# Performance work log

Measured on AMD Instinct MI355X. Metric: run time of the kernel, lower is better.

## Reference

```python
import jax, jax.numpy as jnp
import numpy as np

HIDDEN = 768
NUM_HEADS = 12
HEAD_DIM = HIDDEN // NUM_HEADS


def setup_inputs() -> dict:
    key = jax.random.key(0)
    ks = jax.random.split(key, 10)
    B, S = 4, 2048
    scale = 1.0 / np.sqrt(HIDDEN)
    inp = {
        "hidden_states": jax.random.normal(ks[0], (B, S, HIDDEN), dtype=jnp.float32),
        "attention_mask": jnp.ones((B, S), dtype=jnp.float32),
        "Wq": jax.random.normal(ks[1], (HIDDEN, HIDDEN), dtype=jnp.float32) * scale,
        "bq": jnp.zeros((HIDDEN,), dtype=jnp.float32),
        "Wk": jax.random.normal(ks[2], (HIDDEN, HIDDEN), dtype=jnp.float32) * scale,
        "bk": jnp.zeros((HIDDEN,), dtype=jnp.float32),
        "Wv": jax.random.normal(ks[3], (HIDDEN, HIDDEN), dtype=jnp.float32) * scale,
        "bv": jnp.zeros((HIDDEN,), dtype=jnp.float32),
        "Wo": jax.random.normal(ks[4], (HIDDEN, HIDDEN), dtype=jnp.float32) * scale,
        "bo": jnp.zeros((HIDDEN,), dtype=jnp.float32),
    }
    return inp


def _split_heads(x):
    # [B,S,H] -> [B,nh,S,dh]
    B, S, _ = x.shape
    return x.reshape(B, S, NUM_HEADS, HEAD_DIM).transpose(0, 2, 1, 3)


def reference(hidden_states, attention_mask, Wq, bq, Wk, bk, Wv, bv, Wo, bo):
    # Linear projections (torch nn.Linear: x @ W.T + b; here W stored as [in,out])
    q = _split_heads(hidden_states @ Wq + bq)
    k = _split_heads(hidden_states @ Wk + bk)
    v = _split_heads(hidden_states @ Wv + bv)

    # scores: [B,nh,S,S]
    scores = jnp.einsum("bhqd,bhkd->bhqk", q, k) / np.sqrt(HEAD_DIM).astype(np.float32)

    # outer-product mask: [B,1,S,S], broadcast over heads
    ext = (attention_mask[:, :, None] * attention_mask[:, None, :])[:, None, :, :]
    scores = ext * scores - (1.0 - ext) * 1e9

    probs = jax.nn.softmax(scores, axis=-1)
    ctx = jnp.einsum("bhqk,bhkd->bhqd", probs, v)  # [B,nh,S,dh]
    B, _, S, _ = ctx.shape
    ctx = ctx.transpose(0, 2, 1, 3).reshape(B, S, HIDDEN)
    out = ctx @ Wo + bo
    # torch F.gelu default: exact (erf-based)
    return jax.nn.gelu(out, approximate=False)
```

## Files before the change

### kernel.cpp

```cpp
#include <hip/hip_runtime.h>
#include <math.h>

#define HIDDEN 768
#define NH 12
#define DH 64
#define SEQ 2048
#define BATCH 4

typedef __bf16 bf16;
typedef bf16 bf16x4 __attribute__((ext_vector_type(4)));
typedef bf16 bf16x8 __attribute__((ext_vector_type(8)));
typedef float f32x4 __attribute__((ext_vector_type(4)));

__global__ __launch_bounds__(256) void prep_x(const float* __restrict__ X,
                                              bf16* __restrict__ Xb) {
    const size_t i = ((size_t)blockIdx.x * 256 + threadIdx.x) * 8;
    float4 a = *(const float4*)(X + i);
    float4 b = *(const float4*)(X + i + 4);
    bf16x8 o = {(bf16)a.x, (bf16)a.y, (bf16)a.z, (bf16)a.w,
                (bf16)b.x, (bf16)b.y, (bf16)b.z, (bf16)b.w};
    *(bf16x8*)(Xb + i) = o;
}

__global__ __launch_bounds__(256) void prep_w(const float* __restrict__ Wq,
                                              const float* __restrict__ Wk,
                                              const float* __restrict__ Wv,
                                              const float* __restrict__ Wo,
                                              bf16* __restrict__ Wt,
                                              bf16* __restrict__ Wot_hi,
                                              bf16* __restrict__ Wot_lo) {
    __shared__ float Ts[64][68];
    const int tid = threadIdx.x;
    const int n0 = blockIdx.x * 64, k0 = blockIdx.y * 64, z = blockIdx.z;
    const float* W = (z == 0) ? Wq : (z == 1) ? Wk : (z == 2) ? Wv : Wo;

    {
        const int r = tid >> 2, c = (tid & 3) << 4;
        const float* src = W + (size_t)(k0 + r) * HIDDEN + n0 + c;
#pragma unroll
        for (int j = 0; j < 4; ++j)
            *(float4*)&Ts[r][c + 4 * j] = *(const float4*)(src + 4 * j);
    }
    __syncthreads();

    const int nl = tid >> 2, kc = (tid & 3) << 4;
    float v[16];
#pragma unroll
    for (int j = 0; j < 16; ++j) v[j] = Ts[kc + j][nl];

    if (z < 3) {
        bf16 hi[16];
#pragma unroll
        for (int j = 0; j < 16; ++j) hi[j] = (bf16)v[j];
        const size_t off = (size_t)(z * HIDDEN + n0 + nl) * HIDDEN + k0 + kc;
        *(bf16x8*)(Wt + off) = *(bf16x8*)&hi[0];
        *(bf16x8*)(Wt + off + 8) = *(bf16x8*)&hi[8];
    } else {
        bf16 hi[16], lo[16];
#pragma unroll
        for (int j = 0; j < 16; ++j) {
            hi[j] = (bf16)v[j];
            lo[j] = (bf16)(v[j] - (float)hi[j]);
        }
        const size_t off = (size_t)(n0 + nl) * HIDDEN + k0 + kc;
        *(bf16x8*)(Wot_hi + off) = *(bf16x8*)&hi[0];
        *(bf16x8*)(Wot_hi + off + 8) = *(bf16x8*)&hi[8];
        *(bf16x8*)(Wot_lo + off) = *(bf16x8*)&lo[0];
        *(bf16x8*)(Wot_lo + off + 8) = *(bf16x8*)&lo[8];
    }
}

__global__ __launch_bounds__(256) void gemm_qkv(
    const bf16* __restrict__ Xb, const bf16* __restrict__ Wt,
    const float* __restrict__ bq, const float* __restrict__ bk,
    const float* __restrict__ bv, bf16* __restrict__ q_out,
    bf16* __restrict__ k_out, bf16* __restrict__ v_out) {
    __shared__ bf16 As[128][40];
    __shared__ bf16 Bs[128][40];

    const int tid = threadIdx.x;
    const int ln = tid & 63, wv = tid >> 6;
    const int quad = ln >> 4, l16 = ln & 15;
    const int wm = wv >> 1, wn = wv & 1;
    const int n0 = blockIdx.x * 128, m0 = blockIdx.y * 128;

    f32x4 acc[4][4];
#pragma unroll
    for (int i = 0; i < 4; ++i)
#pragma unroll
        for (int j = 0; j < 4; ++j) acc[i][j] = (f32x4){0.f, 0.f, 0.f, 0.f};

    const int sr = tid >> 1, sc = (tid & 1) << 4;
    const bf16* gA = Xb + (size_t)(m0 + sr) * HIDDEN + sc;
    const bf16* gB = Wt + (size_t)(n0 + sr) * HIDDEN + sc;

    bf16x8 ar0, ar1, br0, br1;
    ar0 = *(const bf16x8*)gA;
    ar1 = *(const bf16x8*)(gA + 8);
    br0 = *(const bf16x8*)gB;
    br1 = *(const bf16x8*)(gB + 8);

    for (int k0 = 0; k0 < HIDDEN; k0 += 32) {
        __syncthreads();
        *(bf16x8*)&As[sr][sc] = ar0;
        *(bf16x8*)&As[sr][sc + 8] = ar1;
        *(bf16x8*)&Bs[sr][sc] = br0;
        *(bf16x8*)&Bs[sr][sc + 8] = br1;
        __syncthreads();
        if (k0 + 32 < HIDDEN) {
            ar0 = *(const bf16x8*)(gA + k0 + 32);
            ar1 = *(const bf16x8*)(gA + k0 + 40);
            br0 = *(const bf16x8*)(gB + k0 + 32);
            br1 = *(const bf16x8*)(gB + k0 + 40);
        }

        bf16x8 ah[4], bh[4];
#pragma unroll
        for (int i = 0; i < 4; ++i) {
            ah[i] = *(bf16x8*)&As[wm * 64 + i * 16 + l16][quad * 8];
            bh[i] = *(bf16x8*)&Bs[wn * 64 + i * 16 + l16][quad * 8];
        }
#pragma unroll
        for (int mi = 0; mi < 4; ++mi)
#pragma unroll
            for (int ni = 0; ni < 4; ++ni)
                acc[mi][ni] = __builtin_amdgcn_mfma_f32_16x16x32_bf16(
                    ah[mi], bh[ni], acc[mi][ni], 0, 0, 0);
    }

    const int nb = n0 + wn * 64;
    const int which = nb / HIDDEN;
    const int nrel = nb - which * HIDDEN;
    const int h = nrel >> 6;

    if (which < 2) {
        const float scale = (which == 0) ? 0.18033688011112042f : 1.0f;
        const float* bias = (which == 0) ? bq : bk;
        bf16* dst = (which == 0) ? q_out : k_out;
#pragma unroll
        for (int ni = 0; ni < 4; ++ni) {
            const int dh = ni * 16 + l16;
            const float bb = bias[nrel + dh];
#pragma unroll
            for (int mi = 0; mi < 4; ++mi)
#pragma unroll
                for (int r = 0; r < 4; ++r) {
                    const int m = m0 + wm * 64 + mi * 16 + quad * 4 + r;
                    const int bi = m >> 11, s = m & (SEQ - 1);
                    dst[(((size_t)(bi * NH + h) * SEQ + s) << 6) + dh] =
                        (bf16)(scale * (acc[mi][ni][r] + bb));
                }
        }
    } else {
        const int bi = m0 >> 11;
        const int sbase = (m0 & (SEQ - 1)) + wm * 64;
#pragma unroll
        for (int ni = 0; ni < 4; ++ni) {
            const int dh = ni * 16 + l16;
            const float bb = bv[nrel + dh];
            bf16* vrow = v_out + ((size_t)(bi * NH + h) * DH + dh) * SEQ;
#pragma unroll
            for (int mi = 0; mi < 4; ++mi) {
                bf16x4 pk = {(bf16)(acc[mi][ni][0] + bb),
                             (bf16)(acc[mi][ni][1] + bb),
                             (bf16)(acc[mi][ni][2] + bb),
                             (bf16)(acc[mi][ni][3] + bb)};
                *(bf16x4*)(vrow + sbase + mi * 16 + quad * 4) = pk;
            }
        }
    }
}

__global__ __launch_bounds__(256) void attn_mfma(const bf16* __restrict__ Q,
                                                 const bf16* __restrict__ K,
                                                 const bf16* __restrict__ Vt,
                                                 const float* __restrict__ mask,
                                                 float* __restrict__ ctx) {
    __shared__ bf16 Ks[64 * 64];
    __shared__ bf16 Vts[64 * 64];
    __shared__ bf16 Ps[128 * 64];
    __shared__ float Ms[SEQ];
    __shared__ int allones_s;

    const int tid = threadIdx.x;
    const int ln = tid & 63, w = tid >> 6;
    const int quad = ln >> 4, l16 = ln & 15;

    const int wg = blockIdx.x;
    const int logical = (wg & 7) * 96 + (wg >> 3);
    const int qt = logical & 15;
    const int h = (logical >> 4) % NH;
    const int b = logical / (16 * NH);

    const size_t bh = (size_t)b * NH + h;
    const bf16* Qp = Q + ((bh * SEQ + (size_t)qt * 128) << 6);
    const bf16* Kp = K + (bh * SEQ << 6);
    const bf16* Vp = Vt + (bh * DH) * SEQ;

    if (tid == 0) allones_s = 1;
    {
        float4 m0 = *(const float4*)(mask + (size_t)b * SEQ + tid * 8);
        float4 m1 = *(const float4*)(mask + (size_t)b * SEQ + tid * 8 + 4);
        *(float4*)&Ms[tid * 8] = m0;
        *(float4*)&Ms[tid * 8 + 4] = m1;
        bool ok = (m0.x == 1.f) & (m0.y == 1.f) & (m0.z == 1.f) &
                  (m0.w == 1.f) & (m1.x == 1.f) & (m1.y == 1.f) &
                  (m1.z == 1.f) & (m1.w == 1.f);
        __syncthreads();
        if (!ok) allones_s = 0;
    }
    __syncthreads();
    const bool fastmask = (allones_s != 0);

    bf16x8 qb[2][2];
#pragma unroll
    for (int qg = 0; qg < 2; ++qg)
#pragma unroll
        for (int hf = 0; hf < 2; ++hf)
            qb[qg][hf] = *(const bf16x8*)(Qp + ((w * 32 + qg * 16 + l16) << 6) +
                                          hf * 32 + quad * 8);
    float mq[2];
#pragma unroll
    for (int qg = 0; qg < 2; ++qg)
        mq[qg] = Ms[qt * 128 + w * 32 + qg * 16 + l16];

    float l_i[2] = {0.f, 0.f};
    f32x4 acc[4][2];
#pragma unroll
    for (int fd = 0; fd < 4; ++fd)
#pragma unroll
        for (int qg = 0; qg < 2; ++qg) acc[fd][qg] = (f32x4){0.f, 0.f, 0.f, 0.f};

    const int sr = tid >> 2, sc = (tid & 3) << 4;
    const int ssw = (sr & 7) << 3;
    const int d0 = sc ^ ssw, d1 = (sc + 8) ^ ssw;
    const bf16* kbase = Kp + ((size_t)sr << 6) + sc;
    const bf16* vbase = Vp + (size_t)sr * SEQ + sc;

    bf16x8 kr0, kr1, vr0, vr1;
    kr0 = *(const bf16x8*)kbase;
    kr1 = *(const bf16x8*)(kbase + 8);
    vr0 = *(const bf16x8*)vbase;
    vr1 = *(const bf16x8*)(vbase + 8);

    for (int kt = 0; kt < SEQ / 64; ++kt) {
        __syncthreads();
        *(bf16x8*)&Ks[sr * 64 + d0] = kr0;
        *(bf16x8*)&Ks[sr * 64 + d1] = kr1;
        *(bf16x8*)&Vts[sr * 64 + d0] = vr0;
        *(bf16x8*)&Vts[sr * 64 + d1] = vr1;
        __syncthreads();
        if (kt + 1 < SEQ / 64) {
            kr0 = *(const bf16x8*)(kbase + ((size_t)(kt + 1) << 12));
            kr1 = *(const bf16x8*)(kbase + ((size_t)(kt + 1) << 12) + 8);
            vr0 = *(const bf16x8*)(vbase + (kt + 1) * 64);
            vr1 = *(const bf16x8*)(vbase + (kt + 1) * 64 + 8);
        }

        const int fsw = (l16 & 7) << 3;
        f32x4 st[4][2];
#pragma unroll
        for (int f = 0; f < 4; ++f) {
            const int krow = (f * 16 + l16) * 64;
            bf16x8 ka0 = *(bf16x8*)&Ks[krow + ((quad * 8) ^ fsw)];
            bf16x8 ka1 = *(bf16x8*)&Ks[krow + ((32 + quad * 8) ^ fsw)];
#pragma unroll
            for (int qg = 0; qg < 2; ++qg) {
                f32x4 c = {0.f, 0.f, 0.f, 0.f};
                c = __builtin_amdgcn_mfma_f32_16x16x32_bf16(ka0, qb[qg][0], c, 0, 0, 0);
                c = __builtin_amdgcn_mfma_f32_16x16x32_bf16(ka1, qb[qg][1], c, 0, 0, 0);
                st[f][qg] = c;
            }
        }

        if (!fastmask) {
#pragma unroll
            for (int f = 0; f < 4; ++f) {
                const float4 mk4 = *(const float4*)&Ms[kt * 64 + f * 16 + quad * 4];
                const float mkk[4] = {mk4.x, mk4.y, mk4.z, mk4.w};
#pragma unroll
                for (int qg = 0; qg < 2; ++qg)
#pragma unroll
                    for (int r = 0; r < 4; ++r) {
                        const float ext = mq[qg] * mkk[r];
                        st[f][qg][r] =
                            ext * st[f][qg][r] - (1.0f - ext) * 1.4426950e9f;
                    }
            }
        }

#pragma unroll
        for (int qg = 0; qg < 2; ++qg) {
            const int row = w * 32 + qg * 16 + l16;
            const int sw = (row & 7) << 3;
            bf16* prow = &Ps[row * 64];
#pragma unroll
            for (int f = 0; f < 4; ++f) {
                float p0 = __builtin_amdgcn_exp2f(st[f][qg][0]);
                float p1 = __builtin_amdgcn_exp2f(st[f][qg][1]);
                float p2 = __builtin_amdgcn_exp2f(st[f][qg][2]);
                float p3 = __builtin_amdgcn_exp2f(st[f][qg][3]);
                l_i[qg] += (p0 + p1) + (p2 + p3);
                bf16x4 pk = {(bf16)p0, (bf16)p1, (bf16)p2, (bf16)p3};
                *(bf16x4*)&prow[(f * 16 + quad * 4) ^ sw] = pk;
            }
        }

        bf16x8 pb[2][2];
#pragma unroll
        for (int qg = 0; qg < 2; ++qg) {
            const int row = w * 32 + qg * 16 + l16;
            const int sw = (row & 7) << 3;
#pragma unroll
            for (int hf = 0; hf < 2; ++hf)
                pb[qg][hf] =
                    *(bf16x8*)&Ps[row * 64 + ((hf * 32 + quad * 8) ^ sw)];
        }
#pragma unroll
        for (int fd = 0; fd < 4; ++fd) {
            const int vrow = (fd * 16 + l16) * 64;
            bf16x8 va0 = *(bf16x8*)&Vts[vrow + ((quad * 8) ^ fsw)];
            bf16x8 va1 = *(bf16x8*)&Vts[vrow + ((32 + quad * 8) ^ fsw)];
#pragma unroll
            for (int qg = 0; qg < 2; ++qg) {
                f32x4 c = acc[fd][qg];
                c = __builtin_amdgcn_mfma_f32_16x16x32_bf16(va0, pb[qg][0], c, 0, 0, 0);
                c = __builtin_amdgcn_mfma_f32_16x16x32_bf16(va1, pb[qg][1], c, 0, 0, 0);
                acc[fd][qg] = c;
            }
        }
    }

#pragma unroll
    for (int qg = 0; qg < 2; ++qg) {
        l_i[qg] += __shfl_xor(l_i[qg], 16);
        l_i[qg] += __shfl_xor(l_i[qg], 32);
    }

#pragma unroll
    for (int qg = 0; qg < 2; ++qg) {
        const float inv = 1.0f / l_i[qg];
        const size_t row = (size_t)b * SEQ + qt * 128 + w * 32 + qg * 16 + l16;
#pragma unroll
        for (int fd = 0; fd < 4; ++fd) {
            float4 o = {acc[fd][qg][0] * inv, acc[fd][qg][1] * inv,
                        acc[fd][qg][2] * inv, acc[fd][qg][3] * inv};
            *(float4*)(ctx + row * HIDDEN + h * 64 + fd * 16 + quad * 4) = o;
        }
    }
}

__global__ __launch_bounds__(256) void gemm_out(const float* __restrict__ ctx,
                                                const bf16* __restrict__ Bhi,
                                                const bf16* __restrict__ Blo,
                                                const float* __restrict__ bo,
                                                float* __restrict__ fout) {
    __shared__ bf16 As_hi[128][40];
    __shared__ bf16 As_lo[128][40];
    __shared__ bf16 Bs_hi[64][40];
    __shared__ bf16 Bs_lo[64][40];

    const int tid = threadIdx.x;
    const int ln = tid & 63, wv = tid >> 6;
    const int quad = ln >> 4, l16 = ln & 15;
    const int wm = wv >> 1, wn = wv & 1;
    const int n0 = blockIdx.x * 64, m0 = blockIdx.y * 128;

    f32x4 acc[4][2];
#pragma unroll
    for (int i = 0; i < 4; ++i)
#pragma unroll
        for (int j = 0; j < 2; ++j) acc[i][j] = (f32x4){0.f, 0.f, 0.f, 0.f};

    const int sra = tid >> 1, sca = (tid & 1) << 4;
    const int srb = tid >> 2, scb = (tid & 3) << 3;
    const float* gA = ctx + (size_t)(m0 + sra) * HIDDEN + sca;
    const bf16* gBh = Bhi + (size_t)(n0 + srb) * HIDDEN + scb;
    const bf16* gBl = Blo + (size_t)(n0 + srb) * HIDDEN + scb;

    float fa[16];
    bf16x8 brh, brl;
#pragma unroll
    for (int j = 0; j < 4; ++j) *(float4*)&fa[4 * j] = *(const float4*)(gA + 4 * j);
    brh = *(const bf16x8*)gBh;
    brl = *(const bf16x8*)gBl;

    for (int k0 = 0; k0 < HIDDEN; k0 += 32) {
        bf16 hi[16], lo[16];
#pragma unroll
        for (int j = 0; j < 16; ++j) {
            hi[j] = (bf16)fa[j];
            lo[j] = (bf16)(fa[j] - (float)hi[j]);
        }
        __syncthreads();
        *(bf16x8*)&As_hi[sra][sca] = *(bf16x8*)&hi[0];
        *(bf16x8*)&As_hi[sra][sca + 8] = *(bf16x8*)&hi[8];
        *(bf16x8*)&As_lo[sra][sca] = *(bf16x8*)&lo[0];
        *(bf16x8*)&As_lo[sra][sca + 8] = *(bf16x8*)&lo[8];
        *(bf16x8*)&Bs_hi[srb][scb] = brh;
        *(bf16x8*)&Bs_lo[srb][scb] = brl;
        __syncthreads();
        if (k0 + 32 < HIDDEN) {
#pragma unroll
            for (int j = 0; j < 4; ++j)
                *(float4*)&fa[4 * j] = *(const float4*)(gA + k0 + 32 + 4 * j);
            brh = *(const bf16x8*)(gBh + k0 + 32);
            brl = *(const bf16x8*)(gBl + k0 + 32);
        }

        bf16x8 ah[4], al[4], bh[2], bl[2];
#pragma unroll
        for (int i = 0; i < 4; ++i) {
            ah[i] = *(bf16x8*)&As_hi[wm * 64 + i * 16 + l16][quad * 8];
            al[i] = *(bf16x8*)&As_lo[wm * 64 + i * 16 + l16][quad * 8];
        }
#pragma unroll
        for (int i = 0; i < 2; ++i) {
            bh[i] = *(bf16x8*)&Bs_hi[wn * 32 + i * 16 + l16][quad * 8];
            bl[i] = *(bf16x8*)&Bs_lo[wn * 32 + i * 16 + l16][quad * 8];
        }
#pragma unroll
        for (int mi = 0; mi < 4; ++mi)
#pragma unroll
            for (int ni = 0; ni < 2; ++ni) {
                f32x4 c = acc[mi][ni];
                c = __builtin_amdgcn_mfma_f32_16x16x32_bf16(ah[mi], bh[ni], c, 0, 0, 0);
                c = __builtin_amdgcn_mfma_f32_16x16x32_bf16(ah[mi], bl[ni], c, 0, 0, 0);
                c = __builtin_amdgcn_mfma_f32_16x16x32_bf16(al[mi], bh[ni], c, 0, 0, 0);
                acc[mi][ni] = c;
            }
    }

#pragma unroll
    for (int ni = 0; ni < 2; ++ni) {
        const int n = n0 + wn * 32 + ni * 16 + l16;
        const float bb = bo[n];
#pragma unroll
        for (int mi = 0; mi < 4; ++mi)
#pragma unroll
            for (int r = 0; r < 4; ++r) {
                const int m = m0 + wm * 64 + mi * 16 + quad * 4 + r;
                float x = acc[mi][ni][r] + bb;
                x = 0.5f * x * (1.0f + erff(x * 0.70710678118654752440f));
                fout[(size_t)m * HIDDEN + n] = x;
            }
    }
}

extern "C" void kernel_launch(void* const* d_in, const int* in_sizes, int n_in,
                              void* d_out, int out_size, void* d_ws, size_t ws_size,
                              hipStream_t stream) {
    const float* X    = (const float*)d_in[0];
    const float* mask = (const float*)d_in[1];
    const float* Wq   = (const float*)d_in[2];
    const float* bq   = (const float*)d_in[3];
    const float* Wk   = (const float*)d_in[4];
    const float* bk   = (const float*)d_in[5];
    const float* Wv   = (const float*)d_in[6];
    const float* bv   = (const float*)d_in[7];
    const float* Wo   = (const float*)d_in[8];
    const float* bo   = (const float*)d_in[9];
    float* out = (float*)d_out;

    char* w = (char*)d_ws;
    const size_t NE = (size_t)BATCH * SEQ * HIDDEN;
    bf16* q_ws   = (bf16*)w;  w += NE * 2;
    bf16* k_ws   = (bf16*)w;  w += NE * 2;
    bf16* vt_ws  = (bf16*)w;  w += NE * 2;
    float* ctx   = (float*)w; w += NE * 4;
    bf16* Xb     = (bf16*)w;  w += NE * 2;
    bf16* Wt     = (bf16*)w;  w += (size_t)3 * HIDDEN * HIDDEN * 2;
    bf16* Wot_hi = (bf16*)w;  w += (size_t)HIDDEN * HIDDEN * 2;
    bf16* Wot_lo = (bf16*)w;  w += (size_t)HIDDEN * HIDDEN * 2;

    prep_x<<<(int)(NE / 2048), 256, 0, stream>>>(X, Xb);
    prep_w<<<dim3(12, 12, 4), 256, 0, stream>>>(Wq, Wk, Wv, Wo, Wt, Wot_hi,
                                                Wot_lo);
    gemm_qkv<<<dim3(18, 64), 256, 0, stream>>>(Xb, Wt, bq, bk, bv, q_ws, k_ws,
                                               vt_ws);
    attn_mfma<<<dim3(16 * NH * BATCH), 256, 0, stream>>>(q_ws, k_ws, vt_ws,
                                                         mask, ctx);
    gemm_out<<<dim3(12, 64), 256, 0, stream>>>(ctx, Wot_hi, Wot_lo, bo, out);
}
```

Before: 268.3 us.

## Load QKV GEMM tiles directly to LDS with swizzle and K=64 steps

```diff
diff --git a/kernel.cpp b/kernel.cpp
--- a/kernel.cpp
+++ b/kernel.cpp
@@ -11,6 +11,12 @@
 typedef bf16 bf16x4 __attribute__((ext_vector_type(4)));
 typedef bf16 bf16x8 __attribute__((ext_vector_type(8)));
 typedef float f32x4 __attribute__((ext_vector_type(4)));
+
+__device__ __forceinline__ void load_lds16(const void* g, void* l) {
+    __builtin_amdgcn_global_load_lds(
+        (__attribute__((address_space(1))) void*)g,
+        (__attribute__((address_space(3))) void*)l, 16, 0, 0);
+}
 
 __global__ __launch_bounds__(256) void prep_x(const float* __restrict__ X,
                                               bf16* __restrict__ Xb) {
@@ -75,8 +81,8 @@
     const float* __restrict__ bq, const float* __restrict__ bk,
     const float* __restrict__ bv, bf16* __restrict__ q_out,
     bf16* __restrict__ k_out, bf16* __restrict__ v_out) {
-    __shared__ bf16 As[128][40];
-    __shared__ bf16 Bs[128][40];
+    __shared__ bf16 As[128 * 64];
+    __shared__ bf16 Bs[128 * 64];
 
     const int tid = threadIdx.x;
     const int ln = tid & 63, wv = tid >> 6;
@@ -90,42 +96,49 @@
 #pragma unroll
         for (int j = 0; j < 4; ++j) acc[i][j] = (f32x4){0.f, 0.f, 0.f, 0.f};
 
-    const int sr = tid >> 1, sc = (tid & 1) << 4;
-    const bf16* gA = Xb + (size_t)(m0 + sr) * HIDDEN + sc;
-    const bf16* gB = Wt + (size_t)(n0 + sr) * HIDDEN + sc;
-
-    bf16x8 ar0, ar1, br0, br1;
-    ar0 = *(const bf16x8*)gA;
-    ar1 = *(const bf16x8*)(gA + 8);
-    br0 = *(const bf16x8*)gB;
-    br1 = *(const bf16x8*)(gB + 8);
-
-    for (int k0 = 0; k0 < HIDDEN; k0 += 32) {
-        __syncthreads();
-        *(bf16x8*)&As[sr][sc] = ar0;
-        *(bf16x8*)&As[sr][sc + 8] = ar1;
-        *(bf16x8*)&Bs[sr][sc] = br0;
-        *(bf16x8*)&Bs[sr][sc + 8] = br1;
-        __syncthreads();
-        if (k0 + 32 < HIDDEN) {
-            ar0 = *(const bf16x8*)(gA + k0 + 32);
-            ar1 = *(const bf16x8*)(gA + k0 + 40);
-            br0 = *(const bf16x8*)(gB + k0 + 32);
-            br1 = *(const bf16x8*)(gB + k0 + 40);
-        }
-
-        bf16x8 ah[4], bh[4];
+    const int r8 = ln >> 3;
+    const int bcol_sw = ((ln & 7) << 4) ^ (r8 << 4);
+    const char* gA =
+        (const char*)Xb + ((size_t)(m0 + wv * 32 + r8) * HIDDEN) * 2 + bcol_sw;
+    const char* gB =
+        (const char*)Wt + ((size_t)(n0 + wv * 32 + r8) * HIDDEN) * 2 + bcol_sw;
+    bf16* As_w = As + (wv * 32) * 64;
+    bf16* Bs_w = Bs + (wv * 32) * 64;
+
+    const int fsw = (l16 & 7) << 4;
+
+    for (int k0 = 0; k0 < HIDDEN; k0 += 64) {
+        __syncthreads();
+#pragma unroll
+        for (int j = 0; j < 4; ++j) {
+            load_lds16(gA + (size_t)k0 * 2 + (size_t)j * (8 * HIDDEN * 2),
+                       As_w + j * 8 * 64);
+            load_lds16(gB + (size_t)k0 * 2 + (size_t)j * (8 * HIDDEN * 2),
+                       Bs_w + j * 8 * 64);
+        }
+        __syncthreads();
+
+        bf16x8 ah[4][2], bh[4][2];
 #pragma unroll
         for (int i = 0; i < 4; ++i) {
-            ah[i] = *(bf16x8*)&As[wm * 64 + i * 16 + l16][quad * 8];
-            bh[i] = *(bf16x8*)&Bs[wn * 64 + i * 16 + l16][quad * 8];
+            const char* ra = (const char*)As + (wm * 64 + i * 16 + l16) * 128;
+            const char* rb = (const char*)Bs + (wn * 64 + i * 16 + l16) * 128;
+            ah[i][0] = *(const bf16x8*)(ra + ((quad * 16) ^ fsw));
+            ah[i][1] = *(const bf16x8*)(ra + ((64 + quad * 16) ^ fsw));
+            bh[i][0] = *(const bf16x8*)(rb + ((quad * 16) ^ fsw));
+            bh[i][1] = *(const bf16x8*)(rb + ((64 + quad * 16) ^ fsw));
         }
 #pragma unroll
         for (int mi = 0; mi < 4; ++mi)
 #pragma unroll
-            for (int ni = 0; ni < 4; ++ni)
-                acc[mi][ni] = __builtin_amdgcn_mfma_f32_16x16x32_bf16(
-                    ah[mi], bh[ni], acc[mi][ni], 0, 0, 0);
+            for (int ni = 0; ni < 4; ++ni) {
+                f32x4 c = acc[mi][ni];
+                c = __builtin_amdgcn_mfma_f32_16x16x32_bf16(ah[mi][0], bh[ni][0],
+                                                            c, 0, 0, 0);
+                c = __builtin_amdgcn_mfma_f32_16x16x32_bf16(ah[mi][1], bh[ni][1],
+                                                            c, 0, 0, 0);
+                acc[mi][ni] = c;
+            }
     }
 
     const int nb = n0 + wn * 64;
```

Measured after the change: 263.1 us. About the same (-1.9%).
